# Optimization experiments

Measured on AMD Instinct MI355X. Metric: run time of the kernel, lower is better.

## Reference

```python
import jax, jax.numpy as jnp
import numpy as np

N, E, T, B = 10000, 100000, 150000, 64
H, EMB = 256, 64
N_ALIGNN, N_GCN = 2, 2
N_CONV = 2 * N_ALIGNN + N_GCN  # 6 EdgeGatedGraphConv layers, all 256->256


def _bn(x, g, b):
    # BatchNorm1d (training-mode batch stats, biased variance), eps=1e-5
    mu = jnp.mean(x, axis=0)
    var = jnp.mean((x - mu) ** 2, axis=0)
    return (x - mu) * jax.lax.rsqrt(var + 1e-5) * g + b


def _mlp(x, W, b, g, bt):
    # MLPLayer: Linear -> BatchNorm1d -> SiLU
    return jax.nn.silu(_bn(x @ W + b, g, bt))


def _egg(x, y, src, dst, W, b, g, bt, n):
    # EdgeGatedGraphConv. W:[5,d,d] = src_gate,dst_gate,edge_gate,src_update,dst_update
    m = (x @ W[0] + b[0])[src] + (x @ W[1] + b[1])[dst] + y @ W[2] + b[2]  # [e,d]
    sigma = jax.nn.sigmoid(m)
    Bh = x @ W[4] + b[4]                                   # dst_update (applied at source, per DGL code)
    num = jax.ops.segment_sum(sigma * Bh[src], dst, num_segments=n)  # sum_sigma_h
    den = jax.ops.segment_sum(sigma, dst, num_segments=n)            # sum_sigma
    h = num / (den + 1e-6)
    xo = x + jax.nn.silu(_bn(x @ W[3] + b[3] + h, g[0], bt[0]))
    yo = y + jax.nn.silu(_bn(m, g[1], bt[1]))
    return xo, yo


def setup_inputs() -> dict:
    key = jax.random.key(0)
    ks = jax.random.split(key, 20)
    nrm = lambda i, shape, s: jax.random.normal(ks[i], shape, dtype=jnp.float32) * s
    inp = {
        'x': nrm(0, (N, 92), 1.0),
        'edge_rbf': nrm(1, (E, 80), 1.0),
        'angle': nrm(2, (T, 40), 1.0),
        'src': jax.random.randint(ks[3], (E,), 0, N),
        'dst': jax.random.randint(ks[4], (E,), 0, N),
        'lg_src': jax.random.randint(ks[5], (T,), 0, E),
        'lg_dst': jax.random.randint(ks[6], (T,), 0, E),
        'graph_ids': jnp.sort(jax.random.randint(ks[7], (N,), 0, B)),
        # atom embedding MLP: 92 -> 256
        'atW': nrm(8, (92, H), 0.05), 'atb': jnp.zeros((H,)), 'atg': jnp.ones((H,)), 'atbt': jnp.zeros((H,)),
        # edge embedding: 80 -> 64 -> 256
        'e1W': nrm(9, (80, EMB), 0.05), 'e1b': jnp.zeros((EMB,)), 'e1g': jnp.ones((EMB,)), 'e1bt': jnp.zeros((EMB,)),
        'e2W': nrm(10, (EMB, H), 0.05), 'e2b': jnp.zeros((H,)), 'e2g': jnp.ones((H,)), 'e2bt': jnp.zeros((H,)),
        # angle (triplet) embedding: 40 -> 64 -> 256
        't1W': nrm(11, (40, EMB), 0.05), 't1b': jnp.zeros((EMB,)), 't1g': jnp.ones((EMB,)), 't1bt': jnp.zeros((EMB,)),
        't2W': nrm(12, (EMB, H), 0.05), 't2b': jnp.zeros((H,)), 't2g': jnp.ones((H,)), 't2bt': jnp.zeros((H,)),
        # 6 EdgeGatedGraphConv layers: 5 linears + 2 BNs each
        'cW': nrm(13, (N_CONV, 5, H, H), 0.05), 'cb': jnp.zeros((N_CONV, 5, H)),
        'cg': jnp.ones((N_CONV, 2, H)), 'cbt': jnp.zeros((N_CONV, 2, H)),
        # readout fc: 256 -> 1
        'fW': nrm(14, (H, 1), 0.05), 'fb': jnp.zeros((1,)),
    }
    return inp


def reference(x, edge_rbf, angle, src, dst, lg_src, lg_dst, graph_ids,
              atW, atb, atg, atbt,
              e1W, e1b, e1g, e1bt, e2W, e2b, e2g, e2bt,
              t1W, t1b, t1g, t1bt, t2W, t2b, t2g, t2bt,
              cW, cb, cg, cbt, fW, fb):
    n, e = x.shape[0], edge_rbf.shape[0]
    h = _mlp(x, atW, atb, atg, atbt)                             # [N,256]
    y = _mlp(_mlp(edge_rbf, e1W, e1b, e1g, e1bt), e2W, e2b, e2g, e2bt)  # [E,256]
    z = _mlp(_mlp(angle, t1W, t1b, t1g, t1bt), t2W, t2b, t2g, t2bt)     # [T,256]
    # ALIGNN layers: alternate crystal-graph and line-graph gated convs
    for i in range(N_ALIGNN):
        j = 2 * i
        h, m = _egg(h, y, src, dst, cW[j], cb[j], cg[j], cbt[j], n)
        y, z = _egg(m, z, lg_src, lg_dst, cW[j + 1], cb[j + 1], cg[j + 1], cbt[j + 1], e)
    # GCN layers on crystal graph only
    for j in range(2 * N_ALIGNN, N_CONV):
        h, y = _egg(h, y, src, dst, cW[j], cb[j], cg[j], cbt[j], n)
    # AvgPooling over nodes per graph, then fc
    counts = jnp.maximum(jax.ops.segment_sum(jnp.ones((n,), h.dtype), graph_ids, num_segments=B), 1.0)
    pooled = jax.ops.segment_sum(h, graph_ids, num_segments=B) / counts[:, None]
    return (pooled @ fW + fb).squeeze(-1)  # [B], link='identity'
```

## Files before the change

kernel.cpp:

```cpp
#include <hip/hip_runtime.h>
#include <math.h>

constexpr int NN = 10000;
constexpr int EE = 100000;
constexpr int TT = 150000;
constexpr int BB = 64;
constexpr int HD = 256;

typedef unsigned short bf;
typedef __attribute__((ext_vector_type(8))) short short8;
typedef __attribute__((ext_vector_type(4))) float f32x4;

static inline int ceildiv(int a, int b) { return (a + b - 1) / b; }
static inline long lmin(long a, long b) { return a < b ? a : b; }

__device__ __forceinline__ float bf2f(bf u) {
  union { unsigned u; float f; } c; c.u = ((unsigned)u) << 16; return c.f;
}
__device__ __forceinline__ bf f2bf(float f) {
  union { float f; unsigned u; } c; c.f = f;
  unsigned r = c.u + 0x7fff + ((c.u >> 16) & 1);
  return (bf)(r >> 16);
}
__device__ __forceinline__ float sigmoidf_(float x) { return 1.f / (1.f + __expf(-x)); }

template <int BN, int EPI, bool STATS>
__global__ __launch_bounds__(256) void k_mgemm(
    const bf* __restrict__ A, int M, int K,
    const bf* __restrict__ WT, const float* __restrict__ bias,
    bf* __restrict__ C, int ldc, int wc0,
    const bf* __restrict__ aggP, int ldg, float* __restrict__ statsP) {
  constexpr int WROWS = 2, WCOLS = 2;
  constexpr int WTM = 64, WTN = BN / WCOLS;
  constexpr int FI = WTM / 16, FJ = WTN / 16;
  constexpr int BKP = 40;
  __shared__ bf As[128 * BKP];
  __shared__ bf Bs[BN * BKP];

  const int t = threadIdx.x;
  const int lane = t & 63, wid = t >> 6;
  const int wr = wid & (WROWS - 1), wc = wid / WROWS;
  const int lq = lane >> 4, lc16 = lane & 15;
  const int row0 = blockIdx.y * 128;
  const int bx = blockIdx.x;
  const int wcolW = wc0 + bx * BN;

  f32x4 acc[FI][FJ] = {};

  for (int k0 = 0; k0 < K; k0 += 32) {
    for (int L = t; L < 512; L += 256) {
      int r = L >> 2, s = L & 3;
      int gr = row0 + r;
      short8 v = {0, 0, 0, 0, 0, 0, 0, 0};
      if (gr < M) v = *(const short8*)&A[(long)gr * K + k0 + s * 8];
      *(short8*)&As[r * BKP + s * 8] = v;
    }
    for (int L = t; L < BN * 4; L += 256) {
      int r = L >> 2, s = L & 3;
      *(short8*)&Bs[r * BKP + s * 8] = *(const short8*)&WT[(long)(wcolW + r) * K + k0 + s * 8];
    }
    __syncthreads();
    short8 af[FI], bfr[FJ];
    int ko = lq * 8;
#pragma unroll
    for (int i = 0; i < FI; i++)
      af[i] = *(const short8*)&As[(wr * WTM + i * 16 + lc16) * BKP + ko];
#pragma unroll
    for (int j = 0; j < FJ; j++)
      bfr[j] = *(const short8*)&Bs[(wc * WTN + j * 16 + lc16) * BKP + ko];
#pragma unroll
    for (int i = 0; i < FI; i++)
#pragma unroll
      for (int j = 0; j < FJ; j++)
        acc[i][j] = __builtin_amdgcn_mfma_f32_16x16x32_bf16(af[i], bfr[j], acc[i][j], 0, 0, 0);
    __syncthreads();
  }

  float bvv[FJ];
#pragma unroll
  for (int j = 0; j < FJ; j++) bvv[j] = bias[wcolW + wc * WTN + j * 16 + lc16];

  float sS[FJ], sQ[FJ];
#pragma unroll
  for (int j = 0; j < FJ; j++) { sS[j] = 0.f; sQ[j] = 0.f; }

#pragma unroll
  for (int i = 0; i < FI; i++) {
#pragma unroll
    for (int r = 0; r < 4; r++) {
      int grow = row0 + wr * WTM + i * 16 + lq * 4 + r;
      if (grow >= M) continue;
      long cbase = (long)grow * ldc + wcolW + wc * WTN;
#pragma unroll
      for (int j = 0; j < FJ; j++) {
        int cc = j * 16 + lc16;
        float v = acc[i][j][r] + bvv[j];
        if (EPI == 3) {
          int rel = bx * BN + wc * WTN + cc;
          v += bf2f(aggP[(long)grow * ldg + rel]);
        }
        C[cbase + cc] = f2bf(v);
        if (STATS) { sS[j] += v; sQ[j] += v * v; }
      }
    }
  }

  if (STATS) {
#pragma unroll
    for (int j = 0; j < FJ; j++) {
      float s = sS[j], q = sQ[j];
      s += __shfl_xor(s, 16); s += __shfl_xor(s, 32);
      q += __shfl_xor(q, 16); q += __shfl_xor(q, 32);
      if (lane < 16) {
        int c = wcolW + wc * WTN + j * 16 + lc16;
        atomicAdd(&statsP[c], s);
        atomicAdd(&statsP[256 + c], q);
      }
    }
  }
}

template <int BN>
__global__ __launch_bounds__(256) void k_mgemm3(
    const bf* __restrict__ Az, const bf* __restrict__ Ay,
    const int* __restrict__ idxS, const int* __restrict__ idxD,
    int M, int K,
    const bf* __restrict__ W2T, const bf* __restrict__ W0T, const bf* __restrict__ W1T,
    const float* __restrict__ b2, const float* __restrict__ b0, const float* __restrict__ b1,
    bf* __restrict__ C, int ldc, float* __restrict__ statsP) {
  constexpr int WROWS = 2, WCOLS = 2;
  constexpr int WTM = 64, WTN = BN / WCOLS;
  constexpr int FI = WTM / 16, FJ = WTN / 16;
  constexpr int BKP = 40;
  __shared__ bf As[128 * BKP];
  __shared__ bf Bs[BN * BKP];

  const int t = threadIdx.x;
  const int lane = t & 63, wid = t >> 6;
  const int wr = wid & (WROWS - 1), wc = wid / WROWS;
  const int lq = lane >> 4, lc16 = lane & 15;
  const int row0 = blockIdx.y * 128;
  const int wcolW = blockIdx.x * BN;

  const int r0 = t >> 2, r1 = 64 + (t >> 2), sld = t & 3;
  const int gr0 = row0 + r0, gr1 = row0 + r1;

  f32x4 acc[FI][FJ] = {};

  for (int mat = 0; mat < 3; mat++) {
    const bf* AS = (mat == 0) ? Az : Ay;
    const bf* WT = (mat == 0) ? W2T : ((mat == 1) ? W0T : W1T);
    long a0 = -1, a1 = -1;
    if (mat == 0) {
      if (gr0 < M) a0 = (long)gr0 * K;
      if (gr1 < M) a1 = (long)gr1 * K;
    } else {
      const int* im = (mat == 1) ? idxS : idxD;
      if (gr0 < M) a0 = (long)im[gr0] * K;
      if (gr1 < M) a1 = (long)im[gr1] * K;
    }
    for (int k0 = 0; k0 < K; k0 += 32) {
      short8 z8 = {0, 0, 0, 0, 0, 0, 0, 0};
      short8 v0 = z8, v1 = z8;
      if (a0 >= 0) v0 = *(const short8*)&AS[a0 + k0 + sld * 8];
      if (a1 >= 0) v1 = *(const short8*)&AS[a1 + k0 + sld * 8];
      *(short8*)&As[r0 * BKP + sld * 8] = v0;
      *(short8*)&As[r1 * BKP + sld * 8] = v1;
      for (int L = t; L < BN * 4; L += 256) {
        int r = L >> 2, s = L & 3;
        *(short8*)&Bs[r * BKP + s * 8] = *(const short8*)&WT[(long)(wcolW + r) * K + k0 + s * 8];
      }
      __syncthreads();
      short8 af[FI], bfr[FJ];
      int ko = lq * 8;
#pragma unroll
      for (int i = 0; i < FI; i++)
        af[i] = *(const short8*)&As[(wr * WTM + i * 16 + lc16) * BKP + ko];
#pragma unroll
      for (int j = 0; j < FJ; j++)
        bfr[j] = *(const short8*)&Bs[(wc * WTN + j * 16 + lc16) * BKP + ko];
#pragma unroll
      for (int i = 0; i < FI; i++)
#pragma unroll
        for (int j = 0; j < FJ; j++)
          acc[i][j] = __builtin_amdgcn_mfma_f32_16x16x32_bf16(af[i], bfr[j], acc[i][j], 0, 0, 0);
      __syncthreads();
    }
  }

  float bvv[FJ];
#pragma unroll
  for (int j = 0; j < FJ; j++) {
    int c = wcolW + wc * WTN + j * 16 + lc16;
    bvv[j] = b2[c] + b0[c] + b1[c];
  }

  float sS[FJ], sQ[FJ];
#pragma unroll
  for (int j = 0; j < FJ; j++) { sS[j] = 0.f; sQ[j] = 0.f; }

#pragma unroll
  for (int i = 0; i < FI; i++) {
#pragma unroll
    for (int r = 0; r < 4; r++) {
      int grow = row0 + wr * WTM + i * 16 + lq * 4 + r;
      if (grow >= M) continue;
      long cbase = (long)grow * ldc + wcolW + wc * WTN;
#pragma unroll
      for (int j = 0; j < FJ; j++) {
        float v = acc[i][j][r] + bvv[j];
        C[cbase + j * 16 + lc16] = f2bf(v);
        sS[j] += v; sQ[j] += v * v;
      }
    }
  }

#pragma unroll
  for (int j = 0; j < FJ; j++) {
    float s = sS[j], q = sQ[j];
    s += __shfl_xor(s, 16); s += __shfl_xor(s, 32);
    q += __shfl_xor(q, 16); q += __shfl_xor(q, 32);
    if (lane < 16) {
      int c = wcolW + wc * WTN + j * 16 + lc16;
      atomicAdd(&statsP[c], s);
      atomicAdd(&statsP[256 + c], q);
    }
  }
}

__global__ __launch_bounds__(256) void k_agg(
    const bf* __restrict__ m, int ldm, int c0, const bf* __restrict__ tD,
    const int* __restrict__ rowptr, const int* __restrict__ eidx,
    const int* __restrict__ srcI, bf* __restrict__ agg, int n) {
  int v = blockIdx.x * 8 + (threadIdx.x >> 5);
  if (v >= n) return;
  int l = threadIdx.x & 31;
  int c = c0 + l * 4;
  int beg = rowptr[v], end = rowptr[v + 1];
  float n0 = 0.f, n1 = 0.f, n2 = 0.f, n3 = 0.f;
  float d0 = 0.f, d1 = 0.f, d2 = 0.f, d3 = 0.f;
  for (int i = beg; i < end; i++) {
    int e = eidx[i];
    ushort4 mv = *(const ushort4*)&m[(long)e * ldm + c];
    ushort4 dv = *(const ushort4*)&tD[(long)srcI[e] * HD + c];
    float s0 = sigmoidf_(bf2f(mv.x)), s1 = sigmoidf_(bf2f(mv.y));
    float s2 = sigmoidf_(bf2f(mv.z)), s3 = sigmoidf_(bf2f(mv.w));
    d0 += s0; d1 += s1; d2 += s2; d3 += s3;
    n0 += s0 * bf2f(dv.x); n1 += s1 * bf2f(dv.y);
    n2 += s2 * bf2f(dv.z); n3 += s3 * bf2f(dv.w);
  }
  *(ushort4*)&agg[(long)v * 128 + l * 4] = make_ushort4(
      f2bf(n0 / (d0 + 1e-6f)), f2bf(n1 / (d1 + 1e-6f)),
      f2bf(n2 / (d2 + 1e-6f)), f2bf(n3 / (d3 + 1e-6f)));
}

__global__ void k_hist(const int* __restrict__ dstI, int ne, int* __restrict__ cnt) {
  int e = blockIdx.x * 256 + threadIdx.x;
  if (e < ne) atomicAdd(&cnt[dstI[e]], 1);
}
__global__ void k_scan1(int* __restrict__ data, int n, int* __restrict__ bsum) {
  __shared__ int sm[256];
  int i = blockIdx.x * 256 + threadIdx.x;
  int v = (i < n) ? data[i] : 0;
  sm[threadIdx.x] = v;
  __syncthreads();
  for (int o = 1; o < 256; o <<= 1) {
    int t = (threadIdx.x >= o) ? sm[threadIdx.x - o] : 0;
    __syncthreads();
    sm[threadIdx.x] += t;
    __syncthreads();
  }
  if (i < n) data[i] = sm[threadIdx.x];
  if (threadIdx.x == 255) bsum[blockIdx.x] = sm[255];
}
__global__ void k_scan2(int* __restrict__ bsum, int nb) {
  if (threadIdx.x == 0) {
    int run = 0;
    for (int i = 0; i < nb; i++) { int t = bsum[i]; bsum[i] = run; run += t; }
  }
}
__global__ void k_scan3(const int* __restrict__ inc, const int* __restrict__ bsum,
                        int n, int* __restrict__ rowptr) {
  int i = blockIdx.x * 256 + threadIdx.x;
  if (i < n) rowptr[i + 1] = inc[i] + bsum[blockIdx.x];
  if (i == 0) rowptr[0] = 0;
}
__global__ void k_fill(const int* __restrict__ dstI, int ne, const int* __restrict__ rowptr,
                       int* __restrict__ fill, int* __restrict__ eidx) {
  int e = blockIdx.x * 256 + threadIdx.x;
  if (e < ne) {
    int v = dstI[e];
    int pos = rowptr[v] + atomicAdd(&fill[v], 1);
    eidx[pos] = e;
  }
}

template <int BN>
__global__ __launch_bounds__(256) void k_vgemm(
    const float* __restrict__ A, int M, int K,
    const float* __restrict__ W, const float* __restrict__ bias,
    bf* __restrict__ C, int Nout) {
  constexpr int BM = 128, BK = 16, TM = 8, TN = BN / 16;
  __shared__ float As[BK][BM + 4];
  __shared__ float Ws[BK][BN + 4];
  const int row0 = blockIdx.y * BM;
  const int col0 = blockIdx.x * BN;
  const int t = threadIdx.x;
  const int tx = t & 15, ty = t >> 4;
  float acc[TM][TN];
#pragma unroll
  for (int i = 0; i < TM; i++)
#pragma unroll
    for (int j = 0; j < TN; j++) acc[i][j] = 0.f;
  const int arow = t >> 4, acol = t & 15;
  constexpr int WR = 256 / BN;
  const int wrow = t / BN, wcol = t % BN;
  for (int k0 = 0; k0 < K; k0 += BK) {
#pragma unroll
    for (int i = 0; i < BM / 16; i++) {
      int r = arow + i * 16;
      int gr = row0 + r, gk = k0 + acol;
      As[acol][r] = (gr < M && gk < K) ? A[(long)gr * K + gk] : 0.f;
    }
#pragma unroll
    for (int i = 0; i < BK / WR; i++) {
      int kk = wrow + i * WR, gk = k0 + kk;
      Ws[kk][wcol] = (gk < K) ? W[(long)gk * Nout + col0 + wcol] : 0.f;
    }
    __syncthreads();
#pragma unroll
    for (int kk = 0; kk < BK; kk++) {
      float a[TM], w[TN];
#pragma unroll
      for (int i = 0; i < TM; i += 4) {
        float4 v = *(const float4*)&As[kk][ty * TM + i];
        a[i] = v.x; a[i + 1] = v.y; a[i + 2] = v.z; a[i + 3] = v.w;
      }
#pragma unroll
      for (int j = 0; j < TN; j += 4) {
        float4 v = *(const float4*)&Ws[kk][tx * TN + j];
        w[j] = v.x; w[j + 1] = v.y; w[j + 2] = v.z; w[j + 3] = v.w;
      }
#pragma unroll
      for (int i = 0; i < TM; i++)
#pragma unroll
        for (int j = 0; j < TN; j++) acc[i][j] = fmaf(a[i], w[j], acc[i][j]);
    }
    __syncthreads();
  }
  float bv[TN];
#pragma unroll
  for (int j = 0; j < TN; j++) bv[j] = bias[col0 + tx * TN + j];
#pragma unroll
  for (int i = 0; i < TM; i++) {
    int gr = row0 + ty * TM + i;
    if (gr >= M) continue;
    long base = (long)gr * Nout + col0 + tx * TN;
#pragma unroll
    for (int j = 0; j < TN; j += 4)
      *(ushort4*)&C[base + j] = make_ushort4(
          f2bf(acc[i][j] + bv[j]), f2bf(acc[i][j + 1] + bv[j + 1]),
          f2bf(acc[i][j + 2] + bv[j + 2]), f2bf(acc[i][j + 3] + bv[j + 3]));
  }
}

__global__ void k_trans(const float* __restrict__ in, bf* __restrict__ out,
                        int K, int N, long instride, long outstride) {
  const float* I = in + (long)blockIdx.z * instride;
  bf* O = out + (long)blockIdx.z * outstride;
  __shared__ float ts[32][33];
  int n0 = blockIdx.x * 32, k0 = blockIdx.y * 32;
  int tn = threadIdx.x & 31, tk = threadIdx.x >> 5;
#pragma unroll
  for (int i = 0; i < 32; i += 8)
    ts[tk + i][tn] = I[(long)(k0 + tk + i) * N + n0 + tn];
  __syncthreads();
#pragma unroll
  for (int i = 0; i < 32; i += 8)
    O[(long)(n0 + tk + i) * K + k0 + tn] = f2bf(ts[tn][tk + i]);
}

__global__ void k_colstats(const bf* __restrict__ X, long M, int ncols,
                           float* __restrict__ sums) {
  int rpb = 256 / ncols;
  int c = threadIdx.x & (ncols - 1);
  int rsub = threadIdx.x / ncols;
  float s = 0.f, q = 0.f;
  for (long r = (long)blockIdx.x * rpb + rsub; r < M; r += (long)gridDim.x * rpb) {
    float v = bf2f(X[r * ncols + c]);
    s += v; q += v * v;
  }
  atomicAdd(&sums[c], s);
  atomicAdd(&sums[ncols + c], q);
}

__global__ void k_bnfin(const float* __restrict__ sums, float invM, int ncols,
                        const float* __restrict__ g, const float* __restrict__ bt,
                        float* __restrict__ sA, float* __restrict__ sB) {
  int c = threadIdx.x;
  if (c < ncols) {
    float mu = sums[c] * invM;
    float var = sums[ncols + c] * invM - mu * mu;
    float a = g[c] * rsqrtf(var + 1e-5f);
    sA[c] = a;
    sB[c] = bt[c] - mu * a;
  }
}

template <bool RES>
__global__ void k_bnsilu(const bf* __restrict__ X, bf* __restrict__ Y, long n4,
                         int mask, const float* __restrict__ sA,
                         const float* __restrict__ sB) {
  long i = (long)blockIdx.x * 256 + threadIdx.x;
  long stride = (long)gridDim.x * 256;
  for (; i < n4; i += stride) {
    ushort4 v = ((const ushort4*)X)[i];
    int c = (int)((i * 4) & mask);
    float t0 = bf2f(v.x) * sA[c + 0] + sB[c + 0];
    float t1 = bf2f(v.y) * sA[c + 1] + sB[c + 1];
    float t2 = bf2f(v.z) * sA[c + 2] + sB[c + 2];
    float t3 = bf2f(v.w) * sA[c + 3] + sB[c + 3];
    float o0 = t0 * sigmoidf_(t0), o1 = t1 * sigmoidf_(t1);
    float o2 = t2 * sigmoidf_(t2), o3 = t3 * sigmoidf_(t3);
    if (RES) {
      ushort4 r4 = ((const ushort4*)Y)[i];
      o0 += bf2f(r4.x); o1 += bf2f(r4.y); o2 += bf2f(r4.z); o3 += bf2f(r4.w);
    }
    ((ushort4*)Y)[i] = make_ushort4(f2bf(o0), f2bf(o1), f2bf(o2), f2bf(o3));
  }
}

__global__ void k_pool(const bf* __restrict__ h, const int* __restrict__ gid,
                       float* __restrict__ pooled, float* __restrict__ cnt, int n) {
  long i = (long)blockIdx.x * 256 + threadIdx.x;
  if (i >= (long)n * HD) return;
  int r = (int)(i >> 8), c = (int)(i & 255);
  int g = gid[r];
  atomicAdd(&pooled[g * HD + c], bf2f(h[i]));
  if (c == 0) atomicAdd(&cnt[g], 1.f);
}

__global__ void k_fc(const float* __restrict__ pooled, const float* __restrict__ cnts,
                     const float* __restrict__ fW, const float* __restrict__ fb,
                     float* __restrict__ out) {
  int b = blockIdx.x, t = threadIdx.x;
  float v = pooled[b * HD + t] * fW[t];
#pragma unroll
  for (int o = 32; o >= 1; o >>= 1) v += __shfl_down(v, o, 64);
  __shared__ float red[4];
  if ((t & 63) == 0) red[t >> 6] = v;
  __syncthreads();
  if (t == 0) out[b] = (red[0] + red[1] + red[2] + red[3]) / fmaxf(cnts[b], 1.f) + fb[0];
}

__global__ void k_diag(float* out, float v) { out[threadIdx.x] = v; }

struct Bufs {
  bf *h, *y, *z, *mb, *tt, *agg, *wTc, *wTe2, *wTt2;
  float *stats, *sA1, *sB1, *sA2, *sB2, *pooled, *cnts;
  int *rpC, *eiC, *cntC, *fillC, *rpL, *eiL, *cntL, *fillL, *bsum;
};

static void build_csr(const int* dstI, int ne, int nbins, int* cnt, int* fill,
                      int* rowptr, int* eidx, int* bsum, hipStream_t stream) {
  hipMemsetAsync(cnt, 0, (size_t)nbins * 4, stream);
  hipMemsetAsync(fill, 0, (size_t)nbins * 4, stream);
  k_hist<<<ceildiv(ne, 256), 256, 0, stream>>>(dstI, ne, cnt);
  int nb = ceildiv(nbins, 256);
  k_scan1<<<nb, 256, 0, stream>>>(cnt, nbins, bsum);
  k_scan2<<<1, 64, 0, stream>>>(bsum, nb);
  k_scan3<<<nb, 256, 0, stream>>>(cnt, bsum, nbins, rowptr);
  k_fill<<<ceildiv(ne, 256), 256, 0, stream>>>(dstI, ne, rowptr, fill, eidx);
}

static void egg_launch(bf* xp, bf* yp, int n, int e, const int* s, const int* d,
                       const int* rp, const int* ei, const bf* WjT, const float* bj,
                       const float* g0, const float* bt0, const float* g1,
                       const float* bt1, const Bufs& B, hipStream_t stream) {
  hipMemsetAsync(B.stats, 0, 1024 * 4, stream);
  k_mgemm<128, 0, false><<<dim3(2, ceildiv(n, 128)), 256, 0, stream>>>(
      xp, n, HD, WjT + 4 * 65536, bj + 4 * 256, B.tt, HD, 0, nullptr, 0, nullptr);
  k_mgemm3<128><<<dim3(2, ceildiv(e, 128)), 256, 0, stream>>>(
      yp, xp, s, d, e, HD, WjT + 2 * 65536, WjT, WjT + 65536,
      bj + 2 * 256, bj, bj + 256, B.mb, HD, B.stats + 512);
  for (int c0 = 0; c0 < HD; c0 += 128) {
    k_agg<<<ceildiv(n, 8), 256, 0, stream>>>(B.mb, HD, c0, B.tt, rp, ei, s, B.agg, n);
    k_mgemm<128, 3, true><<<dim3(1, ceildiv(n, 128)), 256, 0, stream>>>(
        xp, n, HD, WjT + 3 * 65536, bj + 3 * 256, B.tt, HD, c0, B.agg, 128, B.stats);
  }
  k_bnfin<<<1, 256, 0, stream>>>(B.stats + 512, 1.f / (float)e, HD, g1, bt1, B.sA2, B.sB2);
  k_bnfin<<<1, 256, 0, stream>>>(B.stats, 1.f / (float)n, HD, g0, bt0, B.sA1, B.sB1);
  long n4x = (long)n * HD / 4, n4y = (long)e * HD / 4;
  k_bnsilu<true><<<(int)lmin(4096, (n4x + 255) / 256), 256, 0, stream>>>(
      B.tt, xp, n4x, 255, B.sA1, B.sB1);
  k_bnsilu<true><<<(int)lmin(4096, (n4y + 255) / 256), 256, 0, stream>>>(
      B.mb, yp, n4y, 255, B.sA2, B.sB2);
}

extern "C" void kernel_launch(void* const* d_in, const int* in_sizes, int n_in,
                              void* d_out, int out_size, void* d_ws, size_t ws_size,
                              hipStream_t stream) {
  const float* x = (const float*)d_in[0];
  const float* erbf = (const float*)d_in[1];
  const float* ang = (const float*)d_in[2];
  const int* src = (const int*)d_in[3];
  const int* dst = (const int*)d_in[4];
  const int* lsrc = (const int*)d_in[5];
  const int* ldst = (const int*)d_in[6];
  const int* gid = (const int*)d_in[7];
  const float* atW = (const float*)d_in[8];   const float* atb = (const float*)d_in[9];
  const float* atg = (const float*)d_in[10];  const float* atbt = (const float*)d_in[11];
  const float* e1W = (const float*)d_in[12];  const float* e1b = (const float*)d_in[13];
  const float* e1g = (const float*)d_in[14];  const float* e1bt = (const float*)d_in[15];
  const float* e2W = (const float*)d_in[16];  const float* e2b = (const float*)d_in[17];
  const float* e2g = (const float*)d_in[18];  const float* e2bt = (const float*)d_in[19];
  const float* t1W = (const float*)d_in[20];  const float* t1b = (const float*)d_in[21];
  const float* t1g = (const float*)d_in[22];  const float* t1bt = (const float*)d_in[23];
  const float* t2W = (const float*)d_in[24];  const float* t2b = (const float*)d_in[25];
  const float* t2g = (const float*)d_in[26];  const float* t2bt = (const float*)d_in[27];
  const float* cW = (const float*)d_in[28];   const float* cb = (const float*)d_in[29];
  const float* cg = (const float*)d_in[30];   const float* cbt = (const float*)d_in[31];
  const float* fW = (const float*)d_in[32];   const float* fb = (const float*)d_in[33];
  float* out = (float*)d_out;

  const size_t aggB = (size_t)EE * 128 * 2;
  const size_t wTbytes = (30 * 65536 + 2 * 16384) * 2;

  auto al = [](size_t v) { return (v + 255) & ~(size_t)255; };
  size_t base = al((size_t)NN * HD * 2) + al((size_t)EE * HD * 2) + al((size_t)TT * HD * 2)
              + al((size_t)TT * HD * 2) + al((size_t)EE * HD * 2)
              + al(1024 * 4) + 4 * al(256 * 4) + al((size_t)BB * HD * 4) + al(BB * 4)
              + al(10001 * 4) + al(100000 * 4) + al(10000 * 4) + al(10000 * 4)
              + al(100001 * 4) + al(150000 * 4) + al(100000 * 4) + al(100000 * 4)
              + al(512 * 4);
  size_t full = base + al(aggB) + al(wTbytes);

  bool host;
  if (ws_size >= full + 4096)      host = false;
  else if (ws_size >= base + 4096) host = true;
  else { k_diag<<<1, 64, 0, stream>>>(out, 1000.f + (float)(ws_size >> 20)); return; }

  char* p = (char*)d_ws;
  auto take = [&](size_t nb) { void* r = (void*)p; p += (nb + 255) & ~(size_t)255; return r; };
  Bufs B;
  B.h  = (bf*)take((size_t)NN * HD * 2);
  B.y  = (bf*)take((size_t)EE * HD * 2);
  B.z  = (bf*)take((size_t)TT * HD * 2);
  B.mb = (bf*)take((size_t)TT * HD * 2);
  B.tt = (bf*)take((size_t)EE * HD * 2);
  B.stats = (float*)take(1024 * 4);
  B.sA1 = (float*)take(256 * 4); B.sB1 = (float*)take(256 * 4);
  B.sA2 = (float*)take(256 * 4); B.sB2 = (float*)take(256 * 4);
  B.pooled = (float*)take((size_t)BB * HD * 4);
  B.cnts = (float*)take(BB * 4);
  B.rpC = (int*)take(10001 * 4);
  B.eiC = (int*)take(100000 * 4);
  B.cntC = (int*)take(10000 * 4);
  B.fillC = (int*)take(10000 * 4);
  B.rpL = (int*)take(100001 * 4);
  B.eiL = (int*)take(150000 * 4);
  B.cntL = (int*)take(100000 * 4);
  B.fillL = (int*)take(100000 * 4);
  B.bsum = (int*)take(512 * 4);
  if (!host) {
    B.agg = (bf*)take(aggB);
    B.wTc = (bf*)take(wTbytes);
  } else {
    B.agg = (bf*)(void*)d_in[1];
    B.wTc = (bf*)((char*)(void*)d_in[1] + 26000000);
  }
  B.wTe2 = B.wTc + 30 * 65536;
  B.wTt2 = B.wTe2 + 16384;

  bf* et1 = B.mb;
  bf* et2 = B.mb + 6400000;

  auto stats_run = [&](const bf* X, long M, int ncols, const float* g,
                       const float* bt) {
    hipMemsetAsync(B.stats, 0, 2 * ncols * 4, stream);
    k_colstats<<<512, 256, 0, stream>>>(X, M, ncols, B.stats);
    k_bnfin<<<1, 256, 0, stream>>>(B.stats, 1.f / (float)M, ncols, g, bt, B.sA1, B.sB1);
  };
  auto bnsilu_ip = [&](bf* X, long M, int ncols) {
    long n4 = M * ncols / 4;
    k_bnsilu<false><<<(int)lmin(4096, (n4 + 255) / 256), 256, 0, stream>>>(
        X, X, n4, ncols - 1, B.sA1, B.sB1);
  };

  build_csr(dst, EE, NN, B.cntC, B.fillC, B.rpC, B.eiC, B.bsum, stream);
  build_csr(ldst, TT, EE, B.cntL, B.fillL, B.rpL, B.eiL, B.bsum, stream);

  k_vgemm<128><<<dim3(2, ceildiv(NN, 128)), 256, 0, stream>>>(x, NN, 92, atW, atb, B.h, 256);
  stats_run(B.h, NN, 256, atg, atbt);
  bnsilu_ip(B.h, NN, 256);
  k_vgemm<64><<<dim3(1, ceildiv(EE, 128)), 256, 0, stream>>>(erbf, EE, 80, e1W, e1b, et1, 64);
  stats_run(et1, EE, 64, e1g, e1bt);
  bnsilu_ip(et1, EE, 64);
  k_vgemm<64><<<dim3(1, ceildiv(TT, 128)), 256, 0, stream>>>(ang, TT, 40, t1W, t1b, et2, 64);
  stats_run(et2, TT, 64, t1g, t1bt);
  bnsilu_ip(et2, TT, 64);

  k_trans<<<dim3(8, 8, 30), 256, 0, stream>>>(cW, B.wTc, 256, 256, 65536, 65536);
  k_trans<<<dim3(8, 2, 1), 256, 0, stream>>>(e2W, B.wTe2, 64, 256, 0, 0);
  k_trans<<<dim3(8, 2, 1), 256, 0, stream>>>(t2W, B.wTt2, 64, 256, 0, 0);

  hipMemsetAsync(B.stats, 0, 512 * 4, stream);
  k_mgemm<128, 0, true><<<dim3(2, ceildiv(EE, 128)), 256, 0, stream>>>(
      et1, EE, 64, B.wTe2, e2b, B.y, HD, 0, nullptr, 0, B.stats);
  k_bnfin<<<1, 256, 0, stream>>>(B.stats, 1.f / (float)EE, 256, e2g, e2bt, B.sA1, B.sB1);
  bnsilu_ip(B.y, EE, 256);
  hipMemsetAsync(B.stats, 0, 512 * 4, stream);
  k_mgemm<128, 0, true><<<dim3(2, ceildiv(TT, 128)), 256, 0, stream>>>(
      et2, TT, 64, B.wTt2, t2b, B.z, HD, 0, nullptr, 0, B.stats);
  k_bnfin<<<1, 256, 0, stream>>>(B.stats, 1.f / (float)TT, 256, t2g, t2bt, B.sA1, B.sB1);
  bnsilu_ip(B.z, TT, 256);

  auto egg = [&](bf* xp, bf* yp, int n, int e, const int* s, const int* d,
                 const int* rp, const int* ei, int j) {
    const bf* WjT = B.wTc + (size_t)j * 5 * 65536;
    const float* bj = cb + (size_t)j * 5 * HD;
    const float* g0 = cg + (size_t)j * 2 * HD;
    const float* bt0 = cbt + (size_t)j * 2 * HD;
    egg_launch(xp, yp, n, e, s, d, rp, ei, WjT, bj, g0, bt0, g0 + HD, bt0 + HD, B, stream);
  };
  egg(B.h, B.y, NN, EE, src, dst, B.rpC, B.eiC, 0);
  egg(B.y, B.z, EE, TT, lsrc, ldst, B.rpL, B.eiL, 1);
  egg(B.h, B.y, NN, EE, src, dst, B.rpC, B.eiC, 2);
  egg(B.y, B.z, EE, TT, lsrc, ldst, B.rpL, B.eiL, 3);
  egg(B.h, B.y, NN, EE, src, dst, B.rpC, B.eiC, 4);
  egg(B.h, B.y, NN, EE, src, dst, B.rpC, B.eiC, 5);

  hipMemsetAsync(B.pooled, 0, (size_t)BB * HD * 4, stream);
  hipMemsetAsync(B.cnts, 0, BB * 4, stream);
  k_pool<<<ceildiv(NN * HD, 256), 256, 0, stream>>>(B.h, gid, B.pooled, B.cnts, NN);
  k_fc<<<BB, 256, 0, stream>>>(B.pooled, B.cnts, fW, fb, out);
}
```

Measured before the change: 2.714 ms.

## Prefetch GEMM tiles into registers and aggregate all 256 channels in one pass

The two MFMA GEMM kernels now load the next K-tile from global memory into registers while the current tile is being computed, which overlaps global-load latency with MFMA work. They also drop one of the two per-iteration barriers and are specialised to a 128-wide N tile. When workspace allows, the aggregation buffer is widened to the full 256 channels, so each layer runs one k_agg and one fused update GEMM over 2 column blocks instead of two 128-channel passes. The trade-off is more register pressure and a larger workspace, with the old two-pass path kept as a fallback.

```diff
diff --git a/kernel.cpp b/kernel.cpp
--- a/kernel.cpp
+++ b/kernel.cpp
@@ -24,81 +24,88 @@
 }
 __device__ __forceinline__ float sigmoidf_(float x) { return 1.f / (1.f + __expf(-x)); }
 
-template <int BN, int EPI, bool STATS>
+template <int EPI, bool STATS>
 __global__ __launch_bounds__(256) void k_mgemm(
     const bf* __restrict__ A, int M, int K,
     const bf* __restrict__ WT, const float* __restrict__ bias,
     bf* __restrict__ C, int ldc, int wc0,
-    const bf* __restrict__ aggP, int ldg, float* __restrict__ statsP) {
-  constexpr int WROWS = 2, WCOLS = 2;
-  constexpr int WTM = 64, WTN = BN / WCOLS;
-  constexpr int FI = WTM / 16, FJ = WTN / 16;
+    const bf* __restrict__ aggP, int ldg, int aggc0, float* __restrict__ statsP) {
   constexpr int BKP = 40;
   __shared__ bf As[128 * BKP];
-  __shared__ bf Bs[BN * BKP];
+  __shared__ bf Bs[128 * BKP];
 
   const int t = threadIdx.x;
   const int lane = t & 63, wid = t >> 6;
-  const int wr = wid & (WROWS - 1), wc = wid / WROWS;
+  const int wr = wid & 1, wc = wid >> 1;
   const int lq = lane >> 4, lc16 = lane & 15;
   const int row0 = blockIdx.y * 128;
-  const int bx = blockIdx.x;
-  const int wcolW = wc0 + bx * BN;
-
-  f32x4 acc[FI][FJ] = {};
-
-  for (int k0 = 0; k0 < K; k0 += 32) {
-    for (int L = t; L < 512; L += 256) {
-      int r = L >> 2, s = L & 3;
-      int gr = row0 + r;
-      short8 v = {0, 0, 0, 0, 0, 0, 0, 0};
-      if (gr < M) v = *(const short8*)&A[(long)gr * K + k0 + s * 8];
-      *(short8*)&As[r * BKP + s * 8] = v;
-    }
-    for (int L = t; L < BN * 4; L += 256) {
-      int r = L >> 2, s = L & 3;
-      *(short8*)&Bs[r * BKP + s * 8] = *(const short8*)&WT[(long)(wcolW + r) * K + k0 + s * 8];
-    }
+  const int wcolW = wc0 + blockIdx.x * 128;
+
+  const int rs = t >> 2, sld = t & 3;
+  const int gr0 = row0 + rs, gr1 = row0 + 64 + rs;
+  const long ab0 = (gr0 < M) ? (long)gr0 * K : -1;
+  const long ab1 = (gr1 < M) ? (long)gr1 * K : -1;
+  const long wb0 = (long)(wcolW + rs) * K;
+  const long wb1 = (long)(wcolW + 64 + rs) * K;
+  const short8 z8 = {0, 0, 0, 0, 0, 0, 0, 0};
+
+  f32x4 acc[4][4] = {};
+  short8 pa0, pa1, pb0, pb1;
+
+#define FETCH1(k0_) {                                                     \
+    pa0 = (ab0 >= 0) ? *(const short8*)&A[ab0 + (k0_) + sld * 8] : z8;    \
+    pa1 = (ab1 >= 0) ? *(const short8*)&A[ab1 + (k0_) + sld * 8] : z8;    \
+    pb0 = *(const short8*)&WT[wb0 + (k0_) + sld * 8];                     \
+    pb1 = *(const short8*)&WT[wb1 + (k0_) + sld * 8];                     \
+  }
+
+  const int NT = K >> 5;
+  FETCH1(0);
+  for (int kt = 0; kt < NT; kt++) {
+    if (kt) __syncthreads();
+    *(short8*)&As[rs * BKP + sld * 8] = pa0;
+    *(short8*)&As[(64 + rs) * BKP + sld * 8] = pa1;
+    *(short8*)&Bs[rs * BKP + sld * 8] = pb0;
+    *(short8*)&Bs[(64 + rs) * BKP + sld * 8] = pb1;
     __syncthreads();
-    short8 af[FI], bfr[FJ];
+    if (kt + 1 < NT) FETCH1((kt + 1) << 5);
+    short8 af[4], bfr[4];
     int ko = lq * 8;
 #pragma unroll
-    for (int i = 0; i < FI; i++)
-      af[i] = *(const short8*)&As[(wr * WTM + i * 16 + lc16) * BKP + ko];
-#pragma unroll
-    for (int j = 0; j < FJ; j++)
-      bfr[j] = *(const short8*)&Bs[(wc * WTN + j * 16 + lc16) * BKP + ko];
-#pragma unroll
-    for (int i = 0; i < FI; i++)
-#pragma unroll
-      for (int j = 0; j < FJ; j++)
+    for (int i = 0; i < 4; i++)
+      af[i] = *(const short8*)&As[(wr * 64 + i * 16 + lc16) * BKP + ko];
+#pragma unroll
+    for (int j = 0; j < 4; j++)
+      bfr[j] = *(const short8*)&Bs[(wc * 64 + j * 16 + lc16) * BKP + ko];
+#pragma unroll
+    for (int i = 0; i < 4; i++)
+#pragma unroll
+      for (int j = 0; j < 4; j++)
         acc[i][j] = __builtin_amdgcn_mfma_f32_16x16x32_bf16(af[i], bfr[j], acc[i][j], 0, 0, 0);
-    __syncthreads();
-  }
-
-  float bvv[FJ];
-#pragma unroll
-  for (int j = 0; j < FJ; j++) bvv[j] = bias[wcolW + wc * WTN + j * 16 + lc16];
-
-  float sS[FJ], sQ[FJ];
-#pragma unroll
-  for (int j = 0; j < FJ; j++) { sS[j] = 0.f; sQ[j] = 0.f; }
-
-#pragma unroll
-  for (int i = 0; i < FI; i++) {
+  }
+#undef FETCH1
+
+  float bvv[4];
+#pragma unroll
+  for (int j = 0; j < 4; j++) bvv[j] = bias[wcolW + wc * 64 + j * 16 + lc16];
+
+  float sS[4], sQ[4];
+#pragma unroll
+  for (int j = 0; j < 4; j++) { sS[j] = 0.f; sQ[j] = 0.f; }
+
+#pragma unroll
+  for (int i = 0; i < 4; i++) {
 #pragma unroll
     for (int r = 0; r < 4; r++) {
-      int grow = row0 + wr * WTM + i * 16 + lq * 4 + r;
+      int grow = row0 + wr * 64 + i * 16 + lq * 4 + r;
       if (grow >= M) continue;
-      long cbase = (long)grow * ldc + wcolW + wc * WTN;
-#pragma unroll
-      for (int j = 0; j < FJ; j++) {
+      long cbase = (long)grow * ldc + wcolW + wc * 64;
+#pragma unroll
+      for (int j = 0; j < 4; j++) {
         int cc = j * 16 + lc16;
         float v = acc[i][j][r] + bvv[j];
-        if (EPI == 3) {
-          int rel = bx * BN + wc * WTN + cc;
-          v += bf2f(aggP[(long)grow * ldg + rel]);
-        }
+        if (EPI == 3)
+          v += bf2f(aggP[(long)grow * ldg + (wcolW - aggc0) + wc * 64 + cc]);
         C[cbase + cc] = f2bf(v);
         if (STATS) { sS[j] += v; sQ[j] += v * v; }
       }
@@ -107,12 +114,12 @@
 
   if (STATS) {
 #pragma unroll
-    for (int j = 0; j < FJ; j++) {
+    for (int j = 0; j < 4; j++) {
       float s = sS[j], q = sQ[j];
       s += __shfl_xor(s, 16); s += __shfl_xor(s, 32);
       q += __shfl_xor(q, 16); q += __shfl_xor(q, 32);
       if (lane < 16) {
-        int c = wcolW + wc * WTN + j * 16 + lc16;
+        int c = wcolW + wc * 64 + j * 16 + lc16;
         atomicAdd(&statsP[c], s);
         atomicAdd(&statsP[256 + c], q);
       }
@@ -120,94 +127,95 @@
   }
 }
 
-template <int BN>
 __global__ __launch_bounds__(256) void k_mgemm3(
     const bf* __restrict__ Az, const bf* __restrict__ Ay,
-    const int* __restrict__ idxS, const int* __restrict__ idxD,
-    int M, int K,
+    const int* __restrict__ idxS, const int* __restrict__ idxD, int M,
     const bf* __restrict__ W2T, const bf* __restrict__ W0T, const bf* __restrict__ W1T,
     const float* __restrict__ b2, const float* __restrict__ b0, const float* __restrict__ b1,
     bf* __restrict__ C, int ldc, float* __restrict__ statsP) {
-  constexpr int WROWS = 2, WCOLS = 2;
-  constexpr int WTM = 64, WTN = BN / WCOLS;
-  constexpr int FI = WTM / 16, FJ = WTN / 16;
   constexpr int BKP = 40;
   __shared__ bf As[128 * BKP];
-  __shared__ bf Bs[BN * BKP];
+  __shared__ bf Bs[128 * BKP];
 
   const int t = threadIdx.x;
   const int lane = t & 63, wid = t >> 6;
-  const int wr = wid & (WROWS - 1), wc = wid / WROWS;
+  const int wr = wid & 1, wc = wid >> 1;
   const int lq = lane >> 4, lc16 = lane & 15;
   const int row0 = blockIdx.y * 128;
-  const int wcolW = blockIdx.x * BN;
-
-  const int r0 = t >> 2, r1 = 64 + (t >> 2), sld = t & 3;
-  const int gr0 = row0 + r0, gr1 = row0 + r1;
-
-  f32x4 acc[FI][FJ] = {};
-
-  for (int mat = 0; mat < 3; mat++) {
-    const bf* AS = (mat == 0) ? Az : Ay;
-    const bf* WT = (mat == 0) ? W2T : ((mat == 1) ? W0T : W1T);
-    long a0 = -1, a1 = -1;
-    if (mat == 0) {
-      if (gr0 < M) a0 = (long)gr0 * K;
-      if (gr1 < M) a1 = (long)gr1 * K;
-    } else {
-      const int* im = (mat == 1) ? idxS : idxD;
-      if (gr0 < M) a0 = (long)im[gr0] * K;
-      if (gr1 < M) a1 = (long)im[gr1] * K;
-    }
-    for (int k0 = 0; k0 < K; k0 += 32) {
-      short8 z8 = {0, 0, 0, 0, 0, 0, 0, 0};
-      short8 v0 = z8, v1 = z8;
-      if (a0 >= 0) v0 = *(const short8*)&AS[a0 + k0 + sld * 8];
-      if (a1 >= 0) v1 = *(const short8*)&AS[a1 + k0 + sld * 8];
-      *(short8*)&As[r0 * BKP + sld * 8] = v0;
-      *(short8*)&As[r1 * BKP + sld * 8] = v1;
-      for (int L = t; L < BN * 4; L += 256) {
-        int r = L >> 2, s = L & 3;
-        *(short8*)&Bs[r * BKP + s * 8] = *(const short8*)&WT[(long)(wcolW + r) * K + k0 + s * 8];
-      }
-      __syncthreads();
-      short8 af[FI], bfr[FJ];
-      int ko = lq * 8;
-#pragma unroll
-      for (int i = 0; i < FI; i++)
-        af[i] = *(const short8*)&As[(wr * WTM + i * 16 + lc16) * BKP + ko];
-#pragma unroll
-      for (int j = 0; j < FJ; j++)
-        bfr[j] = *(const short8*)&Bs[(wc * WTN + j * 16 + lc16) * BKP + ko];
-#pragma unroll
-      for (int i = 0; i < FI; i++)
-#pragma unroll
-        for (int j = 0; j < FJ; j++)
-          acc[i][j] = __builtin_amdgcn_mfma_f32_16x16x32_bf16(af[i], bfr[j], acc[i][j], 0, 0, 0);
-      __syncthreads();
-    }
-  }
-
-  float bvv[FJ];
-#pragma unroll
-  for (int j = 0; j < FJ; j++) {
-    int c = wcolW + wc * WTN + j * 16 + lc16;
+  const int wcolW = blockIdx.x * 128;
+
+  const int rs = t >> 2, sld = t & 3;
+  const int gr0 = row0 + rs, gr1 = row0 + 64 + rs;
+  const long z0 = (gr0 < M) ? (long)gr0 * HD : -1;
+  const long z1 = (gr1 < M) ? (long)gr1 * HD : -1;
+  const long s0 = (gr0 < M) ? (long)idxS[gr0] * HD : -1;
+  const long s1 = (gr1 < M) ? (long)idxS[gr1] * HD : -1;
+  const long d0 = (gr0 < M) ? (long)idxD[gr0] * HD : -1;
+  const long d1 = (gr1 < M) ? (long)idxD[gr1] * HD : -1;
+  const long wb0 = (long)(wcolW + rs) * HD;
+  const long wb1 = (long)(wcolW + 64 + rs) * HD;
+  const short8 z8 = {0, 0, 0, 0, 0, 0, 0, 0};
+
+  f32x4 acc[4][4] = {};
+  short8 pa0, pa1, pb0, pb1;
+
+#define FETCH3(kt_) {                                                      \
+    int mat_ = (kt_) >> 3, k0_ = ((kt_) & 7) << 5;                         \
+    const bf* Ap_; const bf* Wp_; long a0_, a1_;                           \
+    if (mat_ == 0)      { Ap_ = Az; Wp_ = W2T; a0_ = z0; a1_ = z1; }       \
+    else if (mat_ == 1) { Ap_ = Ay; Wp_ = W0T; a0_ = s0; a1_ = s1; }       \
+    else                { Ap_ = Ay; Wp_ = W1T; a0_ = d0; a1_ = d1; }       \
+    pa0 = (a0_ >= 0) ? *(const short8*)&Ap_[a0_ + k0_ + sld * 8] : z8;     \
+    pa1 = (a1_ >= 0) ? *(const short8*)&Ap_[a1_ + k0_ + sld * 8] : z8;     \
+    pb0 = *(const short8*)&Wp_[wb0 + k0_ + sld * 8];                       \
+    pb1 = *(const short8*)&Wp_[wb1 + k0_ + sld * 8];                       \
+  }
+
+  FETCH3(0);
+  for (int kt = 0; kt < 24; kt++) {
+    if (kt) __syncthreads();
+    *(short8*)&As[rs * BKP + sld * 8] = pa0;
+    *(short8*)&As[(64 + rs) * BKP + sld * 8] = pa1;
+    *(short8*)&Bs[rs * BKP + sld * 8] = pb0;
+    *(short8*)&Bs[(64 + rs) * BKP + sld * 8] = pb1;
+    __syncthreads();
+    if (kt + 1 < 24) FETCH3(kt + 1);
+    short8 af[4], bfr[4];
+    int ko = lq * 8;
+#pragma unroll
+    for (int i = 0; i < 4; i++)
+      af[i] = *(const short8*)&As[(wr * 64 + i * 16 + lc16) * BKP + ko];
+#pragma unroll
+    for (int j = 0; j < 4; j++)
+      bfr[j] = *(const short8*)&Bs[(wc * 64 + j * 16 + lc16) * BKP + ko];
+#pragma unroll
+    for (int i = 0; i < 4; i++)
+#pragma unroll
+      for (int j = 0; j < 4; j++)
+        acc[i][j] = __builtin_amdgcn_mfma_f32_16x16x32_bf16(af[i], bfr[j], acc[i][j], 0, 0, 0);
+  }
+#undef FETCH3
+
+  float bvv[4];
+#pragma unroll
+  for (int j = 0; j < 4; j++) {
+    int c = wcolW + wc * 64 + j * 16 + lc16;
     bvv[j] = b2[c] + b0[c] + b1[c];
   }
 
-  float sS[FJ], sQ[FJ];
-#pragma unroll
-  for (int j = 0; j < FJ; j++) { sS[j] = 0.f; sQ[j] = 0.f; }
-
-#pragma unroll
-  for (int i = 0; i < FI; i++) {
+  float sS[4], sQ[4];
+#pragma unroll
+  for (int j = 0; j < 4; j++) { sS[j] = 0.f; sQ[j] = 0.f; }
+
+#pragma unroll
+  for (int i = 0; i < 4; i++) {
 #pragma unroll
     for (int r = 0; r < 4; r++) {
-      int grow = row0 + wr * WTM + i * 16 + lq * 4 + r;
+      int grow = row0 + wr * 64 + i * 16 + lq * 4 + r;
       if (grow >= M) continue;
-      long cbase = (long)grow * ldc + wcolW + wc * WTN;
-#pragma unroll
-      for (int j = 0; j < FJ; j++) {
+      long cbase = (long)grow * ldc + wcolW + wc * 64;
+#pragma unroll
+      for (int j = 0; j < 4; j++) {
         float v = acc[i][j][r] + bvv[j];
         C[cbase + j * 16 + lc16] = f2bf(v);
         sS[j] += v; sQ[j] += v * v;
@@ -216,25 +224,27 @@
   }
 
 #pragma unroll
-  for (int j = 0; j < FJ; j++) {
+  for (int j = 0; j < 4; j++) {
     float s = sS[j], q = sQ[j];
     s += __shfl_xor(s, 16); s += __shfl_xor(s, 32);
     q += __shfl_xor(q, 16); q += __shfl_xor(q, 32);
     if (lane < 16) {
-      int c = wcolW + wc * WTN + j * 16 + lc16;
+      int c = wcolW + wc * 64 + j * 16 + lc16;
       atomicAdd(&statsP[c], s);
       atomicAdd(&statsP[256 + c], q);
     }
   }
 }
 
+template <int CH>
 __global__ __launch_bounds__(256) void k_agg(
     const bf* __restrict__ m, int ldm, int c0, const bf* __restrict__ tD,
     const int* __restrict__ rowptr, const int* __restrict__ eidx,
-    const int* __restrict__ srcI, bf* __restrict__ agg, int n) {
-  int v = blockIdx.x * 8 + (threadIdx.x >> 5);
+    const int* __restrict__ srcI, bf* __restrict__ agg, int ldg, int n) {
+  constexpr int TPN = CH / 4;
+  int v = blockIdx.x * (256 / TPN) + threadIdx.x / TPN;
   if (v >= n) return;
-  int l = threadIdx.x & 31;
+  int l = threadIdx.x % TPN;
   int c = c0 + l * 4;
   int beg = rowptr[v], end = rowptr[v + 1];
   float n0 = 0.f, n1 = 0.f, n2 = 0.f, n3 = 0.f;
@@ -249,7 +259,7 @@
     n0 += s0 * bf2f(dv.x); n1 += s1 * bf2f(dv.y);
     n2 += s2 * bf2f(dv.z); n3 += s3 * bf2f(dv.w);
   }
-  *(ushort4*)&agg[(long)v * 128 + l * 4] = make_ushort4(
+  *(ushort4*)&agg[(long)v * ldg + l * 4] = make_ushort4(
       f2bf(n0 / (d0 + 1e-6f)), f2bf(n1 / (d1 + 1e-6f)),
       f2bf(n2 / (d2 + 1e-6f)), f2bf(n3 / (d3 + 1e-6f)));
 }
@@ -476,17 +486,25 @@
 static void egg_launch(bf* xp, bf* yp, int n, int e, const int* s, const int* d,
                        const int* rp, const int* ei, const bf* WjT, const float* bj,
                        const float* g0, const float* bt0, const float* g1,
-                       const float* bt1, const Bufs& B, hipStream_t stream) {
+                       const float* bt1, bool host, const Bufs& B, hipStream_t stream) {
   hipMemsetAsync(B.stats, 0, 1024 * 4, stream);
-  k_mgemm<128, 0, false><<<dim3(2, ceildiv(n, 128)), 256, 0, stream>>>(
-      xp, n, HD, WjT + 4 * 65536, bj + 4 * 256, B.tt, HD, 0, nullptr, 0, nullptr);
-  k_mgemm3<128><<<dim3(2, ceildiv(e, 128)), 256, 0, stream>>>(
-      yp, xp, s, d, e, HD, WjT + 2 * 65536, WjT, WjT + 65536,
+  k_mgemm<0, false><<<dim3(2, ceildiv(n, 128)), 256, 0, stream>>>(
+      xp, n, HD, WjT + 4 * 65536, bj + 4 * 256, B.tt, HD, 0, nullptr, 0, 0, nullptr);
+  k_mgemm3<<<dim3(2, ceildiv(e, 128)), 256, 0, stream>>>(
+      yp, xp, s, d, e, WjT + 2 * 65536, WjT, WjT + 65536,
       bj + 2 * 256, bj, bj + 256, B.mb, HD, B.stats + 512);
-  for (int c0 = 0; c0 < HD; c0 += 128) {
-    k_agg<<<ceildiv(n, 8), 256, 0, stream>>>(B.mb, HD, c0, B.tt, rp, ei, s, B.agg, n);
-    k_mgemm<128, 3, true><<<dim3(1, ceildiv(n, 128)), 256, 0, stream>>>(
-        xp, n, HD, WjT + 3 * 65536, bj + 3 * 256, B.tt, HD, c0, B.agg, 128, B.stats);
+  if (!host) {
+    k_agg<256><<<ceildiv(n, 4), 256, 0, stream>>>(B.mb, HD, 0, B.tt, rp, ei, s,
+                                                  B.agg, 256, n);
+    k_mgemm<3, true><<<dim3(2, ceildiv(n, 128)), 256, 0, stream>>>(
+        xp, n, HD, WjT + 3 * 65536, bj + 3 * 256, B.tt, HD, 0, B.agg, 256, 0, B.stats);
+  } else {
+    for (int c0 = 0; c0 < HD; c0 += 128) {
+      k_agg<128><<<ceildiv(n, 8), 256, 0, stream>>>(B.mb, HD, c0, B.tt, rp, ei, s,
+                                                    B.agg, 128, n);
+      k_mgemm<3, true><<<dim3(1, ceildiv(n, 128)), 256, 0, stream>>>(
+          xp, n, HD, WjT + 3 * 65536, bj + 3 * 256, B.tt, HD, c0, B.agg, 128, c0, B.stats);
+    }
   }
   k_bnfin<<<1, 256, 0, stream>>>(B.stats + 512, 1.f / (float)e, HD, g1, bt1, B.sA2, B.sB2);
   k_bnfin<<<1, 256, 0, stream>>>(B.stats, 1.f / (float)n, HD, g0, bt0, B.sA1, B.sB1);
@@ -523,7 +541,7 @@
   const float* fW = (const float*)d_in[32];   const float* fb = (const float*)d_in[33];
   float* out = (float*)d_out;
 
-  const size_t aggB = (size_t)EE * 128 * 2;
+  const size_t aggBfull = (size_t)EE * HD * 2;
   const size_t wTbytes = (30 * 65536 + 2 * 16384) * 2;
 
   auto al = [](size_t v) { return (v + 255) & ~(size_t)255; };
@@ -533,7 +551,7 @@
               + al(10001 * 4) + al(100000 * 4) + al(10000 * 4) + al(10000 * 4)
               + al(100001 * 4) + al(150000 * 4) + al(100000 * 4) + al(100000 * 4)
               + al(512 * 4);
-  size_t full = base + al(aggB) + al(wTbytes);
+  size_t full = base + al(aggBfull) + al(wTbytes);
 
   bool host;
   if (ws_size >= full + 4096)      host = false;
@@ -563,7 +581,7 @@
   B.fillL = (int*)take(100000 * 4);
   B.bsum = (int*)take(512 * 4);
   if (!host) {
-    B.agg = (bf*)take(aggB);
+    B.agg = (bf*)take(aggBfull);
     B.wTc = (bf*)take(wTbytes);
   } else {
     B.agg = (bf*)(void*)d_in[1];
@@ -605,13 +623,13 @@
   k_trans<<<dim3(8, 2, 1), 256, 0, stream>>>(t2W, B.wTt2, 64, 256, 0, 0);
 
   hipMemsetAsync(B.stats, 0, 512 * 4, stream);
-  k_mgemm<128, 0, true><<<dim3(2, ceildiv(EE, 128)), 256, 0, stream>>>(
-      et1, EE, 64, B.wTe2, e2b, B.y, HD, 0, nullptr, 0, B.stats);
+  k_mgemm<0, true><<<dim3(2, ceildiv(EE, 128)), 256, 0, stream>>>(
+      et1, EE, 64, B.wTe2, e2b, B.y, HD, 0, nullptr, 0, 0, B.stats);
   k_bnfin<<<1, 256, 0, stream>>>(B.stats, 1.f / (float)EE, 256, e2g, e2bt, B.sA1, B.sB1);
   bnsilu_ip(B.y, EE, 256);
   hipMemsetAsync(B.stats, 0, 512 * 4, stream);
-  k_mgemm<128, 0, true><<<dim3(2, ceildiv(TT, 128)), 256, 0, stream>>>(
-      et2, TT, 64, B.wTt2, t2b, B.z, HD, 0, nullptr, 0, B.stats);
+  k_mgemm<0, true><<<dim3(2, ceildiv(TT, 128)), 256, 0, stream>>>(
+      et2, TT, 64, B.wTt2, t2b, B.z, HD, 0, nullptr, 0, 0, B.stats);
   k_bnfin<<<1, 256, 0, stream>>>(B.stats, 1.f / (float)TT, 256, t2g, t2bt, B.sA1, B.sB1);
   bnsilu_ip(B.z, TT, 256);
 
@@ -621,7 +639,8 @@
     const float* bj = cb + (size_t)j * 5 * HD;
     const float* g0 = cg + (size_t)j * 2 * HD;
     const float* bt0 = cbt + (size_t)j * 2 * HD;
-    egg_launch(xp, yp, n, e, s, d, rp, ei, WjT, bj, g0, bt0, g0 + HD, bt0 + HD, B, stream);
+    egg_launch(xp, yp, n, e, s, d, rp, ei, WjT, bj, g0, bt0, g0 + HD, bt0 + HD,
+               host, B, stream);
   };
   egg(B.h, B.y, NN, EE, src, dst, B.rpC, B.eiC, 0);
   egg(B.y, B.z, EE, TT, lsrc, ldst, B.rpL, B.eiL, 1);
```

Measured after the change: 2.497 ms. 1.09x faster.
